# Optimization experiments

Hardware: AMD Instinct MI355X
Metric: run time of the kernel (lower is better)

The kernel has to match this reference:

```python
import jax, jax.numpy as jnp
import numpy as np


def setup_inputs() -> dict:
    key = jax.random.key(0)
    k1, k2, k3, k4 = jax.random.split(key, 4)
    S, B, I, H = 2048, 64, 512, 512
    stdv = 1.0 / np.sqrt(H)
    x = jax.random.normal(k1, (S, B, I), dtype=jnp.float32)
    W = jax.random.uniform(k2, (I, 4 * H), dtype=jnp.float32, minval=-stdv, maxval=stdv)
    U = jax.random.uniform(k3, (H, 4 * H), dtype=jnp.float32, minval=-stdv, maxval=stdv)
    bias = jax.random.uniform(k4, (4 * H,), dtype=jnp.float32, minval=-stdv, maxval=stdv)
    return {"x": x, "W": W, "U": U, "bias": bias}


def reference(x, W, U, bias):
    # x: [S, B, I] (batch_first=False). Gates order: i, f, g, o.
    S, B, I = x.shape
    H = U.shape[0]
    # Precompute input projection for all timesteps (batched GEMM).
    xW = jnp.einsum('sbi,ig->sbg', x, W) + bias  # [S, B, 4H]

    def step(carry, xw_t):
        h, c = carry
        gates = xw_t + h @ U  # [B, 4H]
        i_t = jax.nn.sigmoid(gates[:, :H])
        f_t = jax.nn.sigmoid(gates[:, H:2 * H])
        g_t = jnp.tanh(gates[:, 2 * H:3 * H])
        o_t = jax.nn.sigmoid(gates[:, 3 * H:])
        c_new = f_t * c + i_t * g_t
        h_new = o_t * jnp.tanh(c_new)
        return (h_new, c_new), h_new

    h0 = jnp.zeros((B, H), dtype=x.dtype)
    c0 = jnp.zeros((B, H), dtype=x.dtype)
    (h_t, c_t), hidden_seq = jax.lax.scan(step, (h0, c0), xW)
    return hidden_seq, (h_t, c_t)
```

## Files before the change

kernel.cpp:

```cpp
#include <hip/hip_runtime.h>
#include <hip/hip_bf16.h>

#define SLEN 2048
#define BROWS 64
#define IDIM 512
#define HDIM 512
#define BH (BROWS * HDIM)
#define RING 32
#define NREC 64
#define NTOT 256
#define NTHREADS 512

typedef __bf16 bf16x8 __attribute__((ext_vector_type(8)));
typedef float  f32x4  __attribute__((ext_vector_type(4)));
typedef int    i32x4  __attribute__((ext_vector_type(4)));
typedef int    i32x2  __attribute__((ext_vector_type(2)));

__device__ inline unsigned short f2bf(float f) {
  union { float f; unsigned u; } v; v.f = f;
  unsigned r = v.u + 0x7FFFu + ((v.u >> 16) & 1u);
  return (unsigned short)(r >> 16);
}
__device__ inline float bf2f(unsigned short s) {
  union { unsigned u; float f; } v; v.u = ((unsigned)s) << 16;
  return v.f;
}
__device__ inline float sigm(float x) {
  return __builtin_amdgcn_rcpf(1.f + __expf(-x));
}
__device__ inline float tanh_f(float x) {
  float e = __expf(2.f * x);
  return 1.f - 2.f * __builtin_amdgcn_rcpf(e + 1.f);
}

__global__ __launch_bounds__(256) void prep_ct(const float* __restrict__ W,
                                               const float* __restrict__ U,
                                               unsigned short* __restrict__ CT) {
  int k = blockIdx.x;
  const float* src = (k < IDIM) ? (W + (size_t)k * 2048) : (U + (size_t)(k - IDIM) * 2048);
  for (int j = threadIdx.x; j < 2048; j += 256) {
    int gate = j >> 9, hcol = j & 511;
    int w = hcol >> 5, n = (hcol >> 2) & 7, hsub = hcol & 3;
    int row = w * 128 + n * 16 + gate * 4 + hsub;
    CT[(size_t)row * 1024 + k] = f2bf(src[j]);
  }
}

__global__ __launch_bounds__(NTHREADS)
void lstm_fused(const float* __restrict__ x, const float* __restrict__ bias,
                const unsigned short* __restrict__ CT,
                unsigned short* __restrict__ gring,
                unsigned short* __restrict__ hG,
                unsigned* __restrict__ flags,
                unsigned* __restrict__ flags2,
                float* __restrict__ out) {
  const int bid  = blockIdx.x;
  const int tid  = threadIdx.x;
  const int lane = tid & 63;
  const int wid  = tid >> 6;
  const int lg   = lane >> 4;
  const int lc   = lane & 15;

  extern __shared__ char Udyn[];
  __shared__ union {
    struct {
      unsigned short Ast[16 * 512];
      unsigned short Gst[16 * 128];
      unsigned short stag[16][32];
    } r;
    unsigned short Gout[64 * 128];
  } sm;

  if (bid >= NREC) {
    const int wid2 = bid - NREC;
    const int w2 = wid2 & 15;
    const int s  = wid2 >> 4;
    const int rt = wid & 3;
    const int ch = wid >> 2;

    float bias_v[4];
    #pragma unroll
    for (int c4 = 0; c4 < 4; ++c4) {
      int n2 = 4 * ch + c4;
      bias_v[c4] = bias[(lc >> 2) * 512 + w2 * 32 + n2 * 4 + (lc & 3)];
    }

    for (int t = s; t < SLEN; t += 12) {
      if (wid == 0 && t >= RING) {
        unsigned need = (unsigned)(t - RING + 2);
        const unsigned* bp = flags + (size_t)((lane & 3) * 16 + w2) * 16;
        while (__ballot((lane < 4) &&
                        (__hip_atomic_load(bp, __ATOMIC_RELAXED,
                                           __HIP_MEMORY_SCOPE_AGENT) < need)) != 0ull)
          __builtin_amdgcn_s_sleep(16);
      }

      f32x4 acc[4];
      #pragma unroll
      for (int c4 = 0; c4 < 4; ++c4)
        acc[c4] = (f32x4){bias_v[c4], bias_v[c4], bias_v[c4], bias_v[c4]};

      const float* xp = x + ((size_t)t * BROWS + 16 * rt + lc) * IDIM + lg * 8;
      #pragma unroll
      for (int kk = 0; kk < 16; ++kk) {
        f32x4 v0 = *(const f32x4*)(xp + kk * 32);
        f32x4 v1 = *(const f32x4*)(xp + kk * 32 + 4);
        bf16x8 a;
        #pragma unroll
        for (int j = 0; j < 4; ++j) { a[j] = (__bf16)v0[j]; a[4 + j] = (__bf16)v1[j]; }
        #pragma unroll
        for (int c4 = 0; c4 < 4; ++c4) {
          const bf16x8 b = *(const bf16x8*)(CT + (size_t)(w2 * 128 + (4 * ch + c4) * 16 + lc) * 1024
                                            + kk * 32 + lg * 8);
          acc[c4] = __builtin_amdgcn_mfma_f32_16x16x32_bf16(a, b, acc[c4], 0, 0, 0);
        }
      }

      #pragma unroll
      for (int c4 = 0; c4 < 4; ++c4)
        #pragma unroll
        for (int reg = 0; reg < 4; ++reg)
          sm.Gout[(size_t)(16 * rt + 4 * lg + reg) * 128 + (4 * ch + c4) * 16 + lc]
            = f2bf(acc[c4][reg]);
      __syncthreads();

      {
        int row = tid >> 3, cs = (tid & 7) * 16;
        const unsigned short* srcp = sm.Gout + (size_t)row * 128 + cs;
        i32x4 v0 = *(const i32x4*)srcp;
        i32x4 v1 = *(const i32x4*)(srcp + 8);
        unsigned short* d = gring + (size_t)(t & (RING - 1)) * (BROWS * 2048)
                          + (size_t)row * 2048 + w2 * 128 + cs;
        asm volatile("global_store_dwordx4 %0, %1, off sc1" :: "v"(d), "v"(v0) : "memory");
        asm volatile("global_store_dwordx4 %0, %1, off offset:16 sc1" :: "v"(d), "v"(v1) : "memory");
        asm volatile("s_waitcnt vmcnt(0)" ::: "memory");
      }
      __syncthreads();
      if (tid == 0)
        __hip_atomic_store(flags2 + (size_t)((t & (RING - 1)) * 16 + w2) * 16,
                           (unsigned)(t + 1), __ATOMIC_RELAXED, __HIP_MEMORY_SCOPE_AGENT);
    }
    return;
  }

  const int g = bid & 3;
  const int w = bid >> 2;
  const int n = wid;

  #pragma unroll
  for (int i = 0; i < 16; ++i) {
    int idx16 = tid + NTHREADS * i;
    int r = idx16 >> 6, c16 = idx16 & 63;
    i32x4 v = *(const i32x4*)(CT + (size_t)(w * 128 + r) * 1024 + 512 + c16 * 8);
    *(i32x4*)(Udyn + (size_t)r * 1024 + ((c16 * 16) ^ ((r & 7) << 4))) = v;
  }
  __syncthreads();

  float cst[4] = {0.f, 0.f, 0.f, 0.f};
  const bool act = (lc < 4);
  const int hcol = w * 32 + n * 4 + (lc & 3);
  const int sw = (lc & 7) << 4;
  const size_t HS = (size_t)SLEN * BH;

  for (int t = 0; t < SLEN; ++t) {
    if (wid == 0) {
      const unsigned* fpH = flags + (size_t)(g * 16 + (lane & 15)) * 16;
      const unsigned* fpG = flags2 + (size_t)((t & (RING - 1)) * 16 + w) * 16;
      int notok;
      do {
        int ok = 1;
        if (lane < 16) {
          if (t > 0)
            ok = (__hip_atomic_load(fpH, __ATOMIC_RELAXED,
                                    __HIP_MEMORY_SCOPE_AGENT) >= (unsigned)t);
        } else if (lane == 16) {
          ok = (__hip_atomic_load(fpG, __ATOMIC_RELAXED,
                                  __HIP_MEMORY_SCOPE_AGENT) > (unsigned)t);
        }
        notok = !ok;
      } while (__ballot(notok) != 0ull);
    }
    __syncthreads();
    __builtin_amdgcn_sched_barrier(0);

    {
      int grow = tid >> 5, gcs = (tid & 31) * 4;
      const unsigned short* gpG = gring + (size_t)(t & (RING - 1)) * (BROWS * 2048)
                                + ((size_t)16 * g + grow) * 2048 + w * 128 + gcs;
      i32x2 gv;
      i32x4 v0, v1;
      int r = 0, c16 = 0;
      if (t > 0) {
        int idx0 = tid * 2;
        r = idx0 >> 6; c16 = idx0 & 63;
        const unsigned short* gpH = hG + (size_t)((t - 1) & 1) * BH
                                  + ((size_t)16 * g + r) * HDIM + c16 * 8;
        asm volatile("global_load_dwordx4 %0, %2, off sc1\n\t"
                     "global_load_dwordx4 %1, %2, off offset:16 sc1"
                     : "=&v"(v0), "=&v"(v1) : "v"(gpH) : "memory");
      }
      asm volatile("global_load_dwordx2 %0, %1, off sc1" : "=&v"(gv) : "v"(gpG) : "memory");
      asm volatile("s_waitcnt vmcnt(0)" ::: "memory");
      if (t > 0) {
        int rs = (r & 7) << 4;
        char* rowb = (char*)sm.r.Ast + r * 1024;
        *(i32x4*)(rowb + ((c16 * 16) ^ rs)) = v0;
        *(i32x4*)(rowb + (((c16 + 1) * 16) ^ rs)) = v1;
      }
      *(i32x2*)(sm.r.Gst + (size_t)grow * 128 + gcs) = gv;
    }
    __syncthreads();

    f32x4 acc;
    #pragma unroll
    for (int reg = 0; reg < 4; ++reg)
      acc[reg] = bf2f(sm.r.Gst[(size_t)(4 * lg + reg) * 128 + n * 16 + lc]);

    if (t > 0) {
      const char* Ab = (const char*)sm.r.Ast + (size_t)lc * 1024;
      const char* Bb = Udyn + (size_t)(n * 16 + lc) * 1024;
      #pragma unroll
      for (int kk = 0; kk < 16; ++kk) {
        int koff = kk * 64 + lg * 16;
        bf16x8 a = *(const bf16x8*)(Ab + (koff ^ sw));
        bf16x8 b = *(const bf16x8*)(Bb + (koff ^ sw));
        acc = __builtin_amdgcn_mfma_f32_16x16x32_bf16(a, b, acc, 0, 0, 0);
      }
    }

    float hnv[4], cnv[4];
    #pragma unroll
    for (int reg = 0; reg < 4; ++reg) {
      float own = acc[reg];
      float g4  = __shfl_xor(own, 4, 64);
      float g8  = __shfl_xor(own, 8, 64);
      float g12 = __shfl_xor(own, 12, 64);
      float it = sigm(own), ft = sigm(g4), gt = tanh_f(g8), ot = sigm(g12);
      float cn = ft * cst[reg] + it * gt;
      cst[reg] = cn;
      float hn = ot * tanh_f(cn);
      hnv[reg] = hn; cnv[reg] = cn;
      if (act) sm.r.stag[4 * lg + reg][n * 4 + (lc & 3)] = f2bf(hn);
    }
    __syncthreads();

    if (t + 1 < SLEN) {
      if (wid == 0) {
        int row = lane >> 2, ch4 = lane & 3;
        i32x4 hv = *(const i32x4*)((const char*)sm.r.stag + row * 64 + ch4 * 16);
        const unsigned short* d0 = hG + (size_t)(t & 1) * BH
                                 + ((size_t)16 * g + row) * HDIM + w * 32 + ch4 * 8;
        asm volatile("global_store_dwordx4 %0, %1, off sc1"
                     :: "v"(d0), "v"(hv) : "memory");
        asm volatile("s_waitcnt vmcnt(0)" ::: "memory");
        if (lane == 0)
          __hip_atomic_store(flags + (size_t)(g * 16 + w) * 16, (unsigned)(t + 1),
                             __ATOMIC_RELAXED, __HIP_MEMORY_SCOPE_AGENT);
      }
    }

    if (act) {
      #pragma unroll
      for (int reg = 0; reg < 4; ++reg) {
        size_t bglob = (size_t)16 * g + 4 * lg + reg;
        out[(size_t)t * BH + bglob * HDIM + hcol] = hnv[reg];
        if (t == SLEN - 1) {
          out[HS + bglob * HDIM + hcol] = hnv[reg];
          out[HS + BH + bglob * HDIM + hcol] = cnv[reg];
        }
      }
    }
  }
}

extern "C" void kernel_launch(void* const* d_in, const int* in_sizes, int n_in,
                              void* d_out, int out_size, void* d_ws, size_t ws_size,
                              hipStream_t stream) {
  const float* x    = (const float*)d_in[0];
  const float* W    = (const float*)d_in[1];
  const float* U    = (const float*)d_in[2];
  const float* bias = (const float*)d_in[3];
  float* out = (float*)d_out;

  char* p = (char*)d_ws;
  unsigned short* CT    = (unsigned short*)p;                      p += (size_t)2048 * 1024 * 2;
  unsigned short* gring = (unsigned short*)p;                      p += (size_t)RING * BROWS * 2048 * 2;
  unsigned short* hG    = (unsigned short*)p;                      p += (size_t)2 * BH * 2;
  unsigned* flags  = (unsigned*)p;                                 p += 4 * 16 * 16 * 4;
  unsigned* flags2 = (unsigned*)p;

  hipMemsetAsync(flags, 0, (4 * 16 + RING * 16) * 16 * sizeof(unsigned), stream);
  prep_ct<<<1024, 256, 0, stream>>>(W, U, CT);
  lstm_fused<<<NTOT, NTHREADS, 128 * 1024, stream>>>(x, bias, CT, gring, hG, flags, flags2, out);
}
```

Before: 7.329 ms.

## Replace flag-based h handoff with sentinel-polled data in an 8-deep h ring

Result: faster. 6.026 ms (-17.8%).

```diff
diff --git a/kernel.cpp b/kernel.cpp
--- a/kernel.cpp
+++ b/kernel.cpp
@@ -7,6 +7,7 @@
 #define HDIM 512
 #define BH (BROWS * HDIM)
 #define RING 32
+#define HRING 8
 #define NREC 64
 #define NTOT 256
 #define NTHREADS 512
@@ -159,55 +160,62 @@
   float cst[4] = {0.f, 0.f, 0.f, 0.f};
   const bool act = (lc < 4);
   const int hcol = w * 32 + n * 4 + (lc & 3);
-  const int sw = (lc & 7) << 4;
   const size_t HS = (size_t)SLEN * BH;
 
+  const int prow = tid >> 5;
+  const int pc16 = (tid * 2) & 63;
+
   for (int t = 0; t < SLEN; ++t) {
-    if (wid == 0) {
-      const unsigned* fpH = flags + (size_t)(g * 16 + (lane & 15)) * 16;
+    {
       const unsigned* fpG = flags2 + (size_t)((t & (RING - 1)) * 16 + w) * 16;
-      int notok;
+      while (__ballot(__hip_atomic_load(fpG, __ATOMIC_RELAXED,
+                                        __HIP_MEMORY_SCOPE_AGENT)
+                      <= (unsigned)t) != 0ull) {}
+    }
+
+    i32x2 gv;
+    {
+      const unsigned short* gpG = gring + (size_t)(t & (RING - 1)) * (BROWS * 2048)
+                                + ((size_t)16 * g + prow) * 2048 + w * 128 + (tid & 31) * 4;
+      asm volatile("global_load_dwordx2 %0, %1, off sc1" : "=&v"(gv) : "v"(gpG) : "memory");
+    }
+    if (t > 0) {
+      const unsigned short* hp = hG + (size_t)((t - 1) & (HRING - 1)) * BH
+                               + ((size_t)16 * g + prow) * HDIM + pc16 * 8;
+      i32x4 v0, v1;
+      int bad;
       do {
-        int ok = 1;
-        if (lane < 16) {
-          if (t > 0)
-            ok = (__hip_atomic_load(fpH, __ATOMIC_RELAXED,
-                                    __HIP_MEMORY_SCOPE_AGENT) >= (unsigned)t);
-        } else if (lane == 16) {
-          ok = (__hip_atomic_load(fpG, __ATOMIC_RELAXED,
-                                  __HIP_MEMORY_SCOPE_AGENT) > (unsigned)t);
+        asm volatile("global_load_dwordx4 %0, %2, off sc1\n\t"
+                     "global_load_dwordx4 %1, %2, off offset:16 sc1\n\t"
+                     "s_waitcnt vmcnt(0)"
+                     : "=&v"(v0), "=&v"(v1) : "v"(hp) : "memory");
+        bad = 0;
+        #pragma unroll
+        for (int j = 0; j < 4; ++j) {
+          unsigned a = (unsigned)v0[j], b = (unsigned)v1[j];
+          bad |= (int)(((a & 0xFFFFu) == 0xFFFFu) | ((a >> 16) == 0xFFFFu)
+                     | ((b & 0xFFFFu) == 0xFFFFu) | ((b >> 16) == 0xFFFFu));
         }
-        notok = !ok;
-      } while (__ballot(notok) != 0ull);
-    }
-    __syncthreads();
-    __builtin_amdgcn_sched_barrier(0);
-
-    {
-      int grow = tid >> 5, gcs = (tid & 31) * 4;
-      const unsigned short* gpG = gring + (size_t)(t & (RING - 1)) * (BROWS * 2048)
-                                + ((size_t)16 * g + grow) * 2048 + w * 128 + gcs;
-      i32x2 gv;
-      i32x4 v0, v1;
-      int r = 0, c16 = 0;
-      if (t > 0) {
-        int idx0 = tid * 2;
-        r = idx0 >> 6; c16 = idx0 & 63;
-        const unsigned short* gpH = hG + (size_t)((t - 1) & 1) * BH
-                                  + ((size_t)16 * g + r) * HDIM + c16 * 8;
-        asm volatile("global_load_dwordx4 %0, %2, off sc1\n\t"
-                     "global_load_dwordx4 %1, %2, off offset:16 sc1"
-                     : "=&v"(v0), "=&v"(v1) : "v"(gpH) : "memory");
-      }
-      asm volatile("global_load_dwordx2 %0, %1, off sc1" : "=&v"(gv) : "v"(gpG) : "memory");
+      } while (bad);
+      int rs = (prow & 7) << 4;
+      char* rowb = (char*)sm.r.Ast + prow * 1024;
+      *(i32x4*)(rowb + ((pc16 * 16) ^ rs)) = v0;
+      *(i32x4*)(rowb + (((pc16 + 1) * 16) ^ rs)) = v1;
+    } else {
       asm volatile("s_waitcnt vmcnt(0)" ::: "memory");
-      if (t > 0) {
-        int rs = (r & 7) << 4;
-        char* rowb = (char*)sm.r.Ast + r * 1024;
-        *(i32x4*)(rowb + ((c16 * 16) ^ rs)) = v0;
-        *(i32x4*)(rowb + (((c16 + 1) * 16) ^ rs)) = v1;
-      }
-      *(i32x2*)(sm.r.Gst + (size_t)grow * 128 + gcs) = gv;
+    }
+    *(i32x2*)(sm.r.Gst + (size_t)prow * 128 + (tid & 31) * 4) = gv;
+
+    if (wid == 0 && lane == 0)
+      __hip_atomic_store(flags + (size_t)(g * 16 + w) * 16, (unsigned)(t + 1),
+                         __ATOMIC_RELAXED, __HIP_MEMORY_SCOPE_AGENT);
+
+    if (wid == 0 && t >= 2) {
+      int row = lane >> 2, ch4 = lane & 3;
+      unsigned short* dr = hG + (size_t)((t - 2) & (HRING - 1)) * BH
+                         + ((size_t)16 * g + row) * HDIM + w * 32 + ch4 * 8;
+      i32x4 ff = {-1, -1, -1, -1};
+      asm volatile("global_store_dwordx4 %0, %1, off sc1" :: "v"(dr), "v"(ff) : "memory");
     }
     __syncthreads();
 
@@ -217,6 +225,7 @@
       acc[reg] = bf2f(sm.r.Gst[(size_t)(4 * lg + reg) * 128 + n * 16 + lc]);
 
     if (t > 0) {
+      const int sw = (lc & 7) << 4;
       const char* Ab = (const char*)sm.r.Ast + (size_t)lc * 1024;
       const char* Bb = Udyn + (size_t)(n * 16 + lc) * 1024;
       #pragma unroll
@@ -244,19 +253,13 @@
     }
     __syncthreads();
 
-    if (t + 1 < SLEN) {
-      if (wid == 0) {
-        int row = lane >> 2, ch4 = lane & 3;
-        i32x4 hv = *(const i32x4*)((const char*)sm.r.stag + row * 64 + ch4 * 16);
-        const unsigned short* d0 = hG + (size_t)(t & 1) * BH
-                                 + ((size_t)16 * g + row) * HDIM + w * 32 + ch4 * 8;
-        asm volatile("global_store_dwordx4 %0, %1, off sc1"
-                     :: "v"(d0), "v"(hv) : "memory");
-        asm volatile("s_waitcnt vmcnt(0)" ::: "memory");
-        if (lane == 0)
-          __hip_atomic_store(flags + (size_t)(g * 16 + w) * 16, (unsigned)(t + 1),
-                             __ATOMIC_RELAXED, __HIP_MEMORY_SCOPE_AGENT);
-      }
+    if (t + 1 < SLEN && wid == 0) {
+      int row = lane >> 2, ch4 = lane & 3;
+      i32x4 hv = *(const i32x4*)((const char*)sm.r.stag + row * 64 + ch4 * 16);
+      const unsigned short* d0 = hG + (size_t)(t & (HRING - 1)) * BH
+                               + ((size_t)16 * g + row) * HDIM + w * 32 + ch4 * 8;
+      asm volatile("global_store_dwordx4 %0, %1, off sc1"
+                   :: "v"(d0), "v"(hv) : "memory");
     }
 
     if (act) {
@@ -283,12 +286,13 @@
   float* out = (float*)d_out;
 
   char* p = (char*)d_ws;
-  unsigned short* CT    = (unsigned short*)p;                      p += (size_t)2048 * 1024 * 2;
-  unsigned short* gring = (unsigned short*)p;                      p += (size_t)RING * BROWS * 2048 * 2;
-  unsigned short* hG    = (unsigned short*)p;                      p += (size_t)2 * BH * 2;
-  unsigned* flags  = (unsigned*)p;                                 p += 4 * 16 * 16 * 4;
+  unsigned short* CT    = (unsigned short*)p;  p += (size_t)2048 * 1024 * 2;
+  unsigned short* gring = (unsigned short*)p;  p += (size_t)RING * BROWS * 2048 * 2;
+  unsigned short* hG    = (unsigned short*)p;  p += (size_t)HRING * BH * 2;
+  unsigned* flags  = (unsigned*)p;             p += 4 * 16 * 16 * 4;
   unsigned* flags2 = (unsigned*)p;
 
+  hipMemsetAsync(hG, 0xFF, (size_t)HRING * BH * 2, stream);
   hipMemsetAsync(flags, 0, (4 * 16 + RING * 16) * 16 * sizeof(unsigned), stream);
   prep_ct<<<1024, 256, 0, stream>>>(W, U, CT);
   lstm_fused<<<NTOT, NTHREADS, 128 * 1024, stream>>>(x, bias, CT, gring, hG, flags, flags2, out);
```
